# Kernel optimization log

Hardware: AMD Instinct MI355X
Metric: run time of the kernel (lower is better)

The kernel has to match this reference:

```python
import jax, jax.numpy as jnp
import numpy as np

EPS = 1e-5  # torch.nn.CosineSimilarity eps


def setup_inputs() -> dict:
    key = jax.random.key(0)
    x = jax.random.normal(key, (8, 256, 1024), dtype=jnp.float32)
    return {"batch_sequence_tensors": x}


def _worst_sim(x):
    # For every contiguous window [s, e] (1 <= s < e <= S-1, matching
    # exclude_special_tokens + sequential combinatorics), compute
    # min_t in [s,e] cos(mean(x[s:e+1]), x[t]).
    # Trick: dot(sum_{s..e} x_i, x_t) comes from a prefix sum of the Gram
    # matrix, and ||sum_{s..e} x||^2 from a 2-D prefix sum of the Gram matrix,
    # avoiding any [B,S,S,D] intermediates.
    B, S, D = x.shape
    G = jnp.einsum('bsd,btd->bst', x, x)  # [B,S,S] Gram

    # num[b,s,e,t] = sum_{i=s..e} x_i . x_t  via 1-D prefix sum over i
    Cpad = jnp.pad(jnp.cumsum(G, axis=1), ((0, 0), (1, 0), (0, 0)))  # [B,S+1,S]
    num = Cpad[:, 1:, :][:, None, :, :] - Cpad[:, :S, :][:, :, None, :]  # [B,S,S,S]

    # ||sum_{s..e} x||^2 = sum_{i,j in [s,e]} G[i,j] via 2-D prefix sum
    PP = jnp.pad(jnp.cumsum(jnp.cumsum(G, axis=1), axis=2),
                 ((0, 0), (1, 0), (1, 0)))  # [B,S+1,S+1]
    dE = jnp.diagonal(PP[:, 1:, 1:], axis1=1, axis2=2)   # PP[e+1,e+1]  [B,S]
    dS = jnp.diagonal(PP[:, :S, :S], axis1=1, axis2=2)   # PP[s,s]      [B,S]
    cross1 = PP[:, :S, 1:]                               # PP[s,e+1]  axes (s,e)
    cross2 = jnp.swapaxes(PP[:, 1:, :S], 1, 2)           # PP[e+1,s] -> (s,e)
    ssq = dE[:, None, :] + dS[:, :, None] - cross1 - cross2  # [B,S,S]
    sum_norm = jnp.sqrt(jnp.maximum(ssq, 0.0))               # ||sum||

    idx = jnp.arange(S)
    win_len = jnp.maximum(idx[None, :] - idx[:, None] + 1, 1).astype(x.dtype)  # [S,S] (s,e)
    # center = sum / len ; cosine uses the mean exactly as the torch module
    mean_norm = sum_norm / win_len                       # [B,S,S]
    x_norm = jnp.sqrt(jnp.maximum(jnp.diagonal(G, axis1=1, axis2=2), 0.0))  # [B,S]
    denom = jnp.maximum(mean_norm[..., None] * x_norm[:, None, None, :], EPS)
    cos = (num / win_len[None, :, :, None]) / denom      # [B,S,S,S]

    t_in = (idx[None, None, :] >= idx[:, None, None]) & \
           (idx[None, None, :] <= idx[None, :, None])    # [S,S,S] (s,e,t)
    worst = jnp.min(jnp.where(t_in[None], cos, jnp.inf), axis=-1)  # [B,S,S]

    valid = (idx[:, None] >= 1) & (idx[None, :] > idx[:, None])    # 1<=s<e<=S-1
    return jnp.where(valid[None], worst, 0.0)


def reference(batch_sequence_tensors):
    # worst_sim[b,s,e] = min cosine similarity of window mean vs members;
    # the original module's group mask is worst_sim >= threshold (0.9),
    # followed by (data-dependent, non-tensor) subset removal.
    return _worst_sim(batch_sequence_tensors)
```

## Files before the change

### kernel.cpp

```cpp
#include <hip/hip_runtime.h>
#include <stdint.h>

#define NB 8
#define NS 256
#define ND 1024
#define EPSF 1e-5f
#define BIGF 3.0e38f

typedef __attribute__((ext_vector_type(8))) short short8;
typedef __attribute__((ext_vector_type(4))) float f32x4;

__device__ __forceinline__ unsigned short f2bf(float f) {
  unsigned int u = __float_as_uint(f);
  u = (u + 0x7FFFu + ((u >> 16) & 1u)) >> 16;
  return (unsigned short)u;
}

__global__ __launch_bounds__(256) void k_convert(const float* __restrict__ x,
                                                 unsigned short* __restrict__ xb, int n4) {
  int idx = blockIdx.x * blockDim.x + threadIdx.x;
  int stride = gridDim.x * blockDim.x;
  for (int i = idx; i < n4; i += stride) {
    float4 v = reinterpret_cast<const float4*>(x)[i];
    ushort4 o;
    o.x = f2bf(v.x); o.y = f2bf(v.y); o.z = f2bf(v.z); o.w = f2bf(v.w);
    reinterpret_cast<ushort4*>(xb)[i] = o;
  }
}

__global__ __launch_bounds__(256) void k_gemm(const unsigned short* __restrict__ xb,
                                              float* __restrict__ gp) {
  int gw = ((blockIdx.x << 8) + threadIdx.x) >> 6;
  int lane = threadIdx.x & 63;
  int b  = gw & 7;
  int mt = (gw >> 3) & 7;
  int nt = (gw >> 6) & 7;
  int ks = gw >> 9;
  const unsigned short* Ab = xb + ((size_t)b << 18) + ((size_t)(mt << 5) << 10);
  const unsigned short* Bb = xb + ((size_t)b << 18) + ((size_t)(nt << 5) << 10);
  int lr = lane & 15;
  int lk = (lane >> 4) << 3;
  f32x4 acc00 = {0.f,0.f,0.f,0.f}, acc01 = {0.f,0.f,0.f,0.f};
  f32x4 acc10 = {0.f,0.f,0.f,0.f}, acc11 = {0.f,0.f,0.f,0.f};
  int kbase = (ks << 8) + lk;
#pragma unroll 2
  for (int kk = 0; kk < 256; kk += 32) {
    int ko = kbase + kk;
    short8 a0  = *reinterpret_cast<const short8*>(Ab + ((size_t)lr << 10) + ko);
    short8 a1  = *reinterpret_cast<const short8*>(Ab + ((size_t)(16 + lr) << 10) + ko);
    short8 bb0 = *reinterpret_cast<const short8*>(Bb + ((size_t)lr << 10) + ko);
    short8 bb1 = *reinterpret_cast<const short8*>(Bb + ((size_t)(16 + lr) << 10) + ko);
    acc00 = __builtin_amdgcn_mfma_f32_16x16x32_bf16(a0, bb0, acc00, 0, 0, 0);
    acc01 = __builtin_amdgcn_mfma_f32_16x16x32_bf16(a0, bb1, acc01, 0, 0, 0);
    acc10 = __builtin_amdgcn_mfma_f32_16x16x32_bf16(a1, bb0, acc10, 0, 0, 0);
    acc11 = __builtin_amdgcn_mfma_f32_16x16x32_bf16(a1, bb1, acc11, 0, 0, 0);
  }
  float* G = gp + (size_t)ks * (NB * NS * NS) + (size_t)b * NS * NS;
  int r0 = (mt << 5) + ((lane >> 4) << 2);
  int c0 = (nt << 5) + lr;
#pragma unroll
  for (int j = 0; j < 4; ++j) {
    G[(r0 + j) * NS + c0]           = acc00[j];
    G[(r0 + j) * NS + c0 + 16]      = acc01[j];
    G[(r0 + 16 + j) * NS + c0]      = acc10[j];
    G[(r0 + 16 + j) * NS + c0 + 16] = acc11[j];
  }
}

__global__ __launch_bounds__(64) void k_prefix(const float* __restrict__ gp, float* __restrict__ C,
                                               float* __restrict__ DGa, float* __restrict__ IXa) {
  int b = blockIdx.x >> 2;
  int t = ((blockIdx.x & 3) << 6) + threadIdx.x;
  const float* g = gp + (size_t)b * NS * NS;
  const int NP = NB * NS * NS;
  float* Cb = C + (size_t)b * 257 * NS;
  float run = 0.f, mydg = 0.f;
  Cb[t] = 0.f;
  for (int j = 0; j < NS; ++j) {
    int o = j * NS + t;
    float gv = g[o] + g[NP + o] + g[2 * NP + o] + g[3 * NP + o];
    if (j == t) mydg = gv;
    run += gv;
    Cb[(j + 1) * NS + t] = run;
  }
  DGa[b * NS + t] = mydg;
  float xn = sqrtf(fmaxf(mydg, 0.f));
  IXa[b * NS + t] = 1.0f / xn;
}

__global__ __launch_bounds__(256) void k_scan(const float* __restrict__ C, float* __restrict__ S2) {
  int id = blockIdx.x * 4 + (threadIdx.x >> 6);
  int lane = threadIdx.x & 63;
  int b = id / 257;
  int r = id - b * 257;
  const float* Crow = C + ((size_t)b * 257 + r) * NS;
  float* Srow = S2 + ((size_t)b * 257 + r) * 257;
  if (lane == 0) Srow[0] = 0.f;
  float run = 0.f;
  for (int c0 = 0; c0 < NS; c0 += 64) {
    float v = Crow[c0 + lane];
#pragma unroll
    for (int off = 1; off < 64; off <<= 1) {
      float n = __shfl_up(v, off);
      if (lane >= off) v += n;
    }
    Srow[c0 + lane + 1] = run + v;
    run += __shfl(v, 63);
  }
}

__global__ __launch_bounds__(64) void k_wmax(const float* __restrict__ IXa, float* __restrict__ WM) {
  int b = blockIdx.x;
  int lane = threadIdx.x;
  const float* IXb = IXa + b * NS;
  float m = 0.f;
#pragma unroll
  for (int k = 0; k < 4; ++k) m = fmaxf(m, IXb[k * 64 + lane]);
#pragma unroll
  for (int off = 32; off; off >>= 1) m = fmaxf(m, __shfl_xor(m, off));
  if (lane == 0) WM[b] = m;
}

static __device__ const unsigned char kTi[20] = {0,0,0,0,1,1,1,1,2,2,2,3,3,3,4,4,5,5,6,7};
static __device__ const unsigned char kTj[20] = {0,1,2,3,0,1,2,3,1,2,3,1,2,3,2,3,2,3,3,3};

__global__ __launch_bounds__(256) void k_trop(const float* __restrict__ C,
                                              const float* __restrict__ S2,
                                              const float* __restrict__ IXa,
                                              const float* __restrict__ DGa,
                                              const float* __restrict__ WM,
                                              float* __restrict__ out) {
  __shared__ float As[64][36];
  __shared__ float Bs[64][68];
  int blk = blockIdx.x;
  int b = blk / 20;
  int tix = blk - b * 20;
  int i0 = (int)kTi[tix] * 32;
  int j0 = (int)kTj[tix] * 64;
  int tid = threadIdx.x;
  int ii0 = (tid >> 4) << 1;
  int jj0 = (tid & 15) << 2;
  const float* Cb = C + (size_t)b * 257 * NS;
  const float* IXb = IXa + b * NS;
  float acc[8];
#pragma unroll
  for (int k = 0; k < 8; ++k) acc[k] = BIGF;

  int rA = tid >> 4;
  int c4 = (tid & 15) << 2;

  for (int t0 = i0 & ~63; t0 < j0 + 64; t0 += 64) {
    __syncthreads();
    float4 wv = *reinterpret_cast<const float4*>(IXb + t0 + c4);
#pragma unroll
    for (int p = 0; p < 2; ++p) {
      int r = i0 + p * 16 + rA;
      float4 v = *reinterpret_cast<const float4*>(Cb + (size_t)r * NS + t0 + c4);
      As[c4 + 0][p * 16 + rA] = v.x * wv.x;
      As[c4 + 1][p * 16 + rA] = v.y * wv.y;
      As[c4 + 2][p * 16 + rA] = v.z * wv.z;
      As[c4 + 3][p * 16 + rA] = v.w * wv.w;
    }
#pragma unroll
    for (int p = 0; p < 4; ++p) {
      int r = j0 + 1 + p * 16 + rA;
      float4 v = *reinterpret_cast<const float4*>(Cb + (size_t)r * NS + t0 + c4);
      Bs[c4 + 0][p * 16 + rA] = v.x * wv.x;
      Bs[c4 + 1][p * 16 + rA] = v.y * wv.y;
      Bs[c4 + 2][p * 16 + rA] = v.z * wv.z;
      Bs[c4 + 3][p * 16 + rA] = v.w * wv.w;
    }
    __syncthreads();

    int thA = i0 + ii0 - t0;
    int thB = j0 + jj0 - t0;
    if (thA <= -1 && thB >= 63) {
#pragma unroll 4
      for (int tt = 0; tt < 64; ++tt) {
        float2 a = *reinterpret_cast<const float2*>(&As[tt][ii0]);
        float4 bv = *reinterpret_cast<const float4*>(&Bs[tt][jj0]);
        acc[0] = fminf(acc[0], bv.x - a.x);
        acc[1] = fminf(acc[1], bv.y - a.x);
        acc[2] = fminf(acc[2], bv.z - a.x);
        acc[3] = fminf(acc[3], bv.w - a.x);
        acc[4] = fminf(acc[4], bv.x - a.y);
        acc[5] = fminf(acc[5], bv.y - a.y);
        acc[6] = fminf(acc[6], bv.z - a.y);
        acc[7] = fminf(acc[7], bv.w - a.y);
      }
    } else {
#pragma unroll 4
      for (int tt = 0; tt < 64; ++tt) {
        float2 a = *reinterpret_cast<const float2*>(&As[tt][ii0]);
        float4 bv = *reinterpret_cast<const float4*>(&Bs[tt][jj0]);
        float a0 = (tt >= thA)     ? a.x  : -BIGF;
        float a1 = (tt >= thA + 1) ? a.y  : -BIGF;
        float b0 = (tt <= thB)     ? bv.x :  BIGF;
        float b1 = (tt <= thB + 1) ? bv.y :  BIGF;
        float b2 = (tt <= thB + 2) ? bv.z :  BIGF;
        float b3 = (tt <= thB + 3) ? bv.w :  BIGF;
        acc[0] = fminf(acc[0], b0 - a0);
        acc[1] = fminf(acc[1], b1 - a0);
        acc[2] = fminf(acc[2], b2 - a0);
        acc[3] = fminf(acc[3], b3 - a0);
        acc[4] = fminf(acc[4], b0 - a1);
        acc[5] = fminf(acc[5], b1 - a1);
        acc[6] = fminf(acc[6], b2 - a1);
        acc[7] = fminf(acc[7], b3 - a1);
      }
    }
  }

  const float* S2b = S2 + (size_t)b * 257 * 257;
  const float* DGb = DGa + b * NS;
  float wmb = WM[b];
  float* outb = out + ((size_t)b << 16);
#pragma unroll
  for (int k = 0; k < 2; ++k) {
    int i = i0 + ii0 + k;
    if (i < 1) continue;
    float s2ii = S2b[(size_t)i * 257 + i];
#pragma unroll
    for (int l = 0; l < 4; ++l) {
      int j = j0 + jj0 + l;
      if (j <= i) continue;
      float s2jj = S2b[(size_t)(j + 1) * 257 + (j + 1)];
      float s2ij = S2b[(size_t)i * 257 + (j + 1)];
      float s2ji = S2b[(size_t)(j + 1) * 257 + i];
      float ssq = (s2jj - s2ij) - (s2ji - s2ii);
      float sn = sqrtf(fmaxf(ssq, 0.f));
      float win = (float)(j - i + 1);
      float res;
      if (sn >= EPSF * win * wmb) {
        res = acc[k * 4 + l] / sn;
      } else {
        float mn = sn / win;
        float m = BIGF;
        const float* r2 = Cb + (size_t)(j + 1) * NS;
        const float* r1 = Cb + (size_t)i * NS;
        for (int t = i; t <= j; ++t) {
          float num = r2[t] - r1[t];
          float xn = sqrtf(fmaxf(DGb[t], 0.f));
          float den = fmaxf(mn * xn, EPSF);
          m = fminf(m, num / win / den);
        }
        res = m;
      }
      outb[(size_t)i * NS + j] = res;
    }
  }
}

extern "C" void kernel_launch(void* const* d_in, const int* in_sizes, int n_in,
                              void* d_out, int out_size, void* d_ws, size_t ws_size,
                              hipStream_t stream) {
  (void)in_sizes; (void)n_in; (void)ws_size;
  const float* x = (const float*)d_in[0];
  float* out = (float*)d_out;
  char* ws = (char*)d_ws;
  unsigned short* Xb = (unsigned short*)(ws);
  float* Gp  = (float*)(ws + 4194304);
  float* C   = (float*)(ws + 12582912);
  float* S2  = (float*)(ws + 14688256);
  float* DGa = (float*)(ws + 16801824);
  float* IXa = (float*)(ws + 16810016);
  float* WM  = (float*)(ws + 16818208);

  hipMemsetAsync(d_out, 0, (size_t)out_size * sizeof(float), stream);
  k_convert<<<1024, 256, 0, stream>>>(x, Xb, (NB * NS * ND) / 4);
  k_gemm<<<512, 256, 0, stream>>>(Xb, Gp);
  k_prefix<<<32, 64, 0, stream>>>(Gp, C, DGa, IXa);
  k_scan<<<514, 256, 0, stream>>>(C, S2);
  k_wmax<<<8, 64, 0, stream>>>(IXa, WM);
  k_trop<<<160, 256, 0, stream>>>(C, S2, IXa, DGa, WM, out);
}
```

Measured before the change: 127.3 us.

## Compute prefix-sum Gram directly via GEMM of prefix-summed X, fuse auxiliary kernels

Replaces the Gram-then-column-prefix pipeline with a prefix sum over the sequence of X in bf16 (Y), then a GEMM Y·X^T that yields the prefix Gram directly. This removes the serial k_prefix kernel. Row norms move into the convert kernel, the weight max moves into k_trop, and the output memset is replaced by explicit zero writes in lower-triangle tiles. The GEMM split-K drops from 4 to 2. Rounding the running prefix sum to bf16 loses precision on large accumulated sums, and the new k_ypfx is a serial scan over 256 rows done by only 32 blocks.

```diff
diff --git a/kernel.cpp b/kernel.cpp
--- a/kernel.cpp
+++ b/kernel.cpp
@@ -15,36 +15,67 @@
   u = (u + 0x7FFFu + ((u >> 16) & 1u)) >> 16;
   return (unsigned short)u;
 }
+__device__ __forceinline__ float bf2f(unsigned short u) {
+  return __uint_as_float((unsigned int)u << 16);
+}
 
 __global__ __launch_bounds__(256) void k_convert(const float* __restrict__ x,
-                                                 unsigned short* __restrict__ xb, int n4) {
-  int idx = blockIdx.x * blockDim.x + threadIdx.x;
-  int stride = gridDim.x * blockDim.x;
-  for (int i = idx; i < n4; i += stride) {
-    float4 v = reinterpret_cast<const float4*>(x)[i];
-    ushort4 o;
-    o.x = f2bf(v.x); o.y = f2bf(v.y); o.z = f2bf(v.z); o.w = f2bf(v.w);
-    reinterpret_cast<ushort4*>(xb)[i] = o;
-  }
-}
-
-__global__ __launch_bounds__(256) void k_gemm(const unsigned short* __restrict__ xb,
-                                              float* __restrict__ gp) {
+                                                 unsigned short* __restrict__ xb,
+                                                 float* __restrict__ DGa,
+                                                 float* __restrict__ IXa) {
+  int row = blockIdx.x * 4 + (threadIdx.x >> 6);
+  int lane = threadIdx.x & 63;
+  size_t base = (size_t)row * ND;
+  float sq = 0.f;
+#pragma unroll
+  for (int c = 0; c < 4; ++c) {
+    size_t o = base + c * 256 + lane * 4;
+    float4 v = *reinterpret_cast<const float4*>(x + o);
+    ushort4 ob;
+    ob.x = f2bf(v.x); ob.y = f2bf(v.y); ob.z = f2bf(v.z); ob.w = f2bf(v.w);
+    *reinterpret_cast<ushort4*>(xb + o) = ob;
+    sq += v.x * v.x + v.y * v.y + v.z * v.z + v.w * v.w;
+  }
+#pragma unroll
+  for (int off = 32; off; off >>= 1) sq += __shfl_xor(sq, off);
+  if (lane == 0) {
+    DGa[row] = sq;
+    IXa[row] = 1.0f / sqrtf(sq);
+  }
+}
+
+__global__ __launch_bounds__(256) void k_ypfx(const unsigned short* __restrict__ xb,
+                                              unsigned short* __restrict__ yb) {
+  int gid = blockIdx.x * 256 + threadIdx.x;
+  int b = gid >> 10;
+  int d = gid & 1023;
+  const unsigned short* xr = xb + ((size_t)b << 18) + d;
+  unsigned short* yr = yb + ((size_t)b << 18) + d;
+  float run = 0.f;
+  for (int s = 0; s < NS; ++s) {
+    run += bf2f(xr[(size_t)s * ND]);
+    yr[(size_t)s * ND] = f2bf(run);
+  }
+}
+
+__global__ __launch_bounds__(256) void k_gemmC(const unsigned short* __restrict__ yb,
+                                               const unsigned short* __restrict__ xb,
+                                               float* __restrict__ cp) {
   int gw = ((blockIdx.x << 8) + threadIdx.x) >> 6;
   int lane = threadIdx.x & 63;
   int b  = gw & 7;
   int mt = (gw >> 3) & 7;
   int nt = (gw >> 6) & 7;
-  int ks = gw >> 9;
-  const unsigned short* Ab = xb + ((size_t)b << 18) + ((size_t)(mt << 5) << 10);
+  int ks = (gw >> 9) & 1;
+  const unsigned short* Ab = yb + ((size_t)b << 18) + ((size_t)(mt << 5) << 10);
   const unsigned short* Bb = xb + ((size_t)b << 18) + ((size_t)(nt << 5) << 10);
   int lr = lane & 15;
   int lk = (lane >> 4) << 3;
   f32x4 acc00 = {0.f,0.f,0.f,0.f}, acc01 = {0.f,0.f,0.f,0.f};
   f32x4 acc10 = {0.f,0.f,0.f,0.f}, acc11 = {0.f,0.f,0.f,0.f};
-  int kbase = (ks << 8) + lk;
+  int kbase = (ks << 9) + lk;
 #pragma unroll 2
-  for (int kk = 0; kk < 256; kk += 32) {
+  for (int kk = 0; kk < 512; kk += 32) {
     int ko = kbase + kk;
     short8 a0  = *reinterpret_cast<const short8*>(Ab + ((size_t)lr << 10) + ko);
     short8 a1  = *reinterpret_cast<const short8*>(Ab + ((size_t)(16 + lr) << 10) + ko);
@@ -55,7 +86,7 @@
     acc10 = __builtin_amdgcn_mfma_f32_16x16x32_bf16(a1, bb0, acc10, 0, 0, 0);
     acc11 = __builtin_amdgcn_mfma_f32_16x16x32_bf16(a1, bb1, acc11, 0, 0, 0);
   }
-  float* G = gp + (size_t)ks * (NB * NS * NS) + (size_t)b * NS * NS;
+  float* G = cp + (size_t)ks * (NB * NS * NS) + ((size_t)b << 16);
   int r0 = (mt << 5) + ((lane >> 4) << 2);
   int c0 = (nt << 5) + lr;
 #pragma unroll
@@ -67,38 +98,22 @@
   }
 }
 
-__global__ __launch_bounds__(64) void k_prefix(const float* __restrict__ gp, float* __restrict__ C,
-                                               float* __restrict__ DGa, float* __restrict__ IXa) {
-  int b = blockIdx.x >> 2;
-  int t = ((blockIdx.x & 3) << 6) + threadIdx.x;
-  const float* g = gp + (size_t)b * NS * NS;
-  const int NP = NB * NS * NS;
-  float* Cb = C + (size_t)b * 257 * NS;
-  float run = 0.f, mydg = 0.f;
-  Cb[t] = 0.f;
-  for (int j = 0; j < NS; ++j) {
-    int o = j * NS + t;
-    float gv = g[o] + g[NP + o] + g[2 * NP + o] + g[3 * NP + o];
-    if (j == t) mydg = gv;
-    run += gv;
-    Cb[(j + 1) * NS + t] = run;
-  }
-  DGa[b * NS + t] = mydg;
-  float xn = sqrtf(fmaxf(mydg, 0.f));
-  IXa[b * NS + t] = 1.0f / xn;
-}
-
-__global__ __launch_bounds__(256) void k_scan(const float* __restrict__ C, float* __restrict__ S2) {
+__global__ __launch_bounds__(256) void k_scan(const float* __restrict__ cp,
+                                              float* __restrict__ C, float* __restrict__ S2) {
   int id = blockIdx.x * 4 + (threadIdx.x >> 6);
   int lane = threadIdx.x & 63;
   int b = id / 257;
   int r = id - b * 257;
-  const float* Crow = C + ((size_t)b * 257 + r) * NS;
+  float* Crow = C + ((size_t)b * 257 + r) * NS;
   float* Srow = S2 + ((size_t)b * 257 + r) * 257;
+  const float* p0 = cp + (((size_t)b << 8) + (r - 1)) * NS;
+  const float* p1 = p0 + (size_t)NB * NS * NS;
   if (lane == 0) Srow[0] = 0.f;
   float run = 0.f;
   for (int c0 = 0; c0 < NS; c0 += 64) {
-    float v = Crow[c0 + lane];
+    float v = 0.f;
+    if (r > 0) v = p0[c0 + lane] + p1[c0 + lane];
+    Crow[c0 + lane] = v;
 #pragma unroll
     for (int off = 1; off < 64; off <<= 1) {
       float n = __shfl_up(v, off);
@@ -108,40 +123,43 @@
     run += __shfl(v, 63);
   }
 }
-
-__global__ __launch_bounds__(64) void k_wmax(const float* __restrict__ IXa, float* __restrict__ WM) {
-  int b = blockIdx.x;
-  int lane = threadIdx.x;
-  const float* IXb = IXa + b * NS;
-  float m = 0.f;
-#pragma unroll
-  for (int k = 0; k < 4; ++k) m = fmaxf(m, IXb[k * 64 + lane]);
-#pragma unroll
-  for (int off = 32; off; off >>= 1) m = fmaxf(m, __shfl_xor(m, off));
-  if (lane == 0) WM[b] = m;
-}
-
-static __device__ const unsigned char kTi[20] = {0,0,0,0,1,1,1,1,2,2,2,3,3,3,4,4,5,5,6,7};
-static __device__ const unsigned char kTj[20] = {0,1,2,3,0,1,2,3,1,2,3,1,2,3,2,3,2,3,3,3};
 
 __global__ __launch_bounds__(256) void k_trop(const float* __restrict__ C,
                                               const float* __restrict__ S2,
                                               const float* __restrict__ IXa,
                                               const float* __restrict__ DGa,
-                                              const float* __restrict__ WM,
                                               float* __restrict__ out) {
   __shared__ float As[64][36];
   __shared__ float Bs[64][68];
+  __shared__ float wred[4];
   int blk = blockIdx.x;
-  int b = blk / 20;
-  int tix = blk - b * 20;
-  int i0 = (int)kTi[tix] * 32;
-  int j0 = (int)kTj[tix] * 64;
+  int b = blk >> 5;
+  int tix = blk & 31;
+  int i0 = (tix >> 2) << 5;
+  int j0 = (tix & 3) << 6;
   int tid = threadIdx.x;
+  float* outb = out + ((size_t)b << 16);
+
+  if (i0 >= j0 + 63) {
+    float4 z = {0.f, 0.f, 0.f, 0.f};
+    float* p = outb + (size_t)(i0 + (tid >> 3)) * NS + j0 + ((tid & 7) << 3);
+    reinterpret_cast<float4*>(p)[0] = z;
+    reinterpret_cast<float4*>(p)[1] = z;
+    return;
+  }
+
+  const float* Cb = C + (size_t)b * 257 * NS;
+  const float* IXb = IXa + b * NS;
+
+  float wv0 = IXb[tid];
+#pragma unroll
+  for (int off = 32; off; off >>= 1) wv0 = fmaxf(wv0, __shfl_xor(wv0, off));
+  if ((tid & 63) == 0) wred[tid >> 6] = wv0;
+  __syncthreads();
+  float wmb = fmaxf(fmaxf(wred[0], wred[1]), fmaxf(wred[2], wred[3]));
+
   int ii0 = (tid >> 4) << 1;
   int jj0 = (tid & 15) << 2;
-  const float* Cb = C + (size_t)b * 257 * NS;
-  const float* IXb = IXa + b * NS;
   float acc[8];
 #pragma unroll
   for (int k = 0; k < 8; ++k) acc[k] = BIGF;
@@ -213,64 +231,63 @@
 
   const float* S2b = S2 + (size_t)b * 257 * 257;
   const float* DGb = DGa + b * NS;
-  float wmb = WM[b];
-  float* outb = out + ((size_t)b << 16);
 #pragma unroll
   for (int k = 0; k < 2; ++k) {
     int i = i0 + ii0 + k;
-    if (i < 1) continue;
+    float o4[4];
     float s2ii = S2b[(size_t)i * 257 + i];
 #pragma unroll
     for (int l = 0; l < 4; ++l) {
       int j = j0 + jj0 + l;
-      if (j <= i) continue;
-      float s2jj = S2b[(size_t)(j + 1) * 257 + (j + 1)];
-      float s2ij = S2b[(size_t)i * 257 + (j + 1)];
-      float s2ji = S2b[(size_t)(j + 1) * 257 + i];
-      float ssq = (s2jj - s2ij) - (s2ji - s2ii);
-      float sn = sqrtf(fmaxf(ssq, 0.f));
-      float win = (float)(j - i + 1);
-      float res;
-      if (sn >= EPSF * win * wmb) {
-        res = acc[k * 4 + l] / sn;
-      } else {
-        float mn = sn / win;
-        float m = BIGF;
-        const float* r2 = Cb + (size_t)(j + 1) * NS;
-        const float* r1 = Cb + (size_t)i * NS;
-        for (int t = i; t <= j; ++t) {
-          float num = r2[t] - r1[t];
-          float xn = sqrtf(fmaxf(DGb[t], 0.f));
-          float den = fmaxf(mn * xn, EPSF);
-          m = fminf(m, num / win / den);
+      float res = 0.f;
+      if (i >= 1 && j > i) {
+        float s2jj = S2b[(size_t)(j + 1) * 257 + (j + 1)];
+        float s2ij = S2b[(size_t)i * 257 + (j + 1)];
+        float s2ji = S2b[(size_t)(j + 1) * 257 + i];
+        float ssq = (s2jj - s2ij) - (s2ji - s2ii);
+        float sn = sqrtf(fmaxf(ssq, 0.f));
+        float win = (float)(j - i + 1);
+        if (sn >= EPSF * win * wmb) {
+          res = acc[k * 4 + l] / sn;
+        } else {
+          float mn = sn / win;
+          float m = BIGF;
+          const float* r2 = Cb + (size_t)(j + 1) * NS;
+          const float* r1 = Cb + (size_t)i * NS;
+          for (int t = i; t <= j; ++t) {
+            float num = r2[t] - r1[t];
+            float xn = sqrtf(fmaxf(DGb[t], 0.f));
+            float den = fmaxf(mn * xn, EPSF);
+            m = fminf(m, num / win / den);
+          }
+          res = m;
         }
-        res = m;
       }
-      outb[(size_t)i * NS + j] = res;
-    }
+      o4[l] = res;
+    }
+    float4 st = {o4[0], o4[1], o4[2], o4[3]};
+    *reinterpret_cast<float4*>(outb + (size_t)i * NS + j0 + jj0) = st;
   }
 }
 
 extern "C" void kernel_launch(void* const* d_in, const int* in_sizes, int n_in,
                               void* d_out, int out_size, void* d_ws, size_t ws_size,
                               hipStream_t stream) {
-  (void)in_sizes; (void)n_in; (void)ws_size;
+  (void)in_sizes; (void)n_in; (void)ws_size; (void)out_size;
   const float* x = (const float*)d_in[0];
   float* out = (float*)d_out;
   char* ws = (char*)d_ws;
   unsigned short* Xb = (unsigned short*)(ws);
-  float* Gp  = (float*)(ws + 4194304);
+  unsigned short* Yb = (unsigned short*)(ws + 4194304);
+  float* Cp  = (float*)(ws + 8388608);
   float* C   = (float*)(ws + 12582912);
   float* S2  = (float*)(ws + 14688256);
   float* DGa = (float*)(ws + 16801824);
   float* IXa = (float*)(ws + 16810016);
-  float* WM  = (float*)(ws + 16818208);
-
-  hipMemsetAsync(d_out, 0, (size_t)out_size * sizeof(float), stream);
-  k_convert<<<1024, 256, 0, stream>>>(x, Xb, (NB * NS * ND) / 4);
-  k_gemm<<<512, 256, 0, stream>>>(Xb, Gp);
-  k_prefix<<<32, 64, 0, stream>>>(Gp, C, DGa, IXa);
-  k_scan<<<514, 256, 0, stream>>>(C, S2);
-  k_wmax<<<8, 64, 0, stream>>>(IXa, WM);
-  k_trop<<<160, 256, 0, stream>>>(C, S2, IXa, DGa, WM, out);
-}
+
+  k_convert<<<512, 256, 0, stream>>>(x, Xb, DGa, IXa);
+  k_ypfx<<<32, 256, 0, stream>>>(Xb, Yb);
+  k_gemmC<<<256, 256, 0, stream>>>(Yb, Xb, Cp);
+  k_scan<<<514, 256, 0, stream>>>(Cp, C, S2);
+  k_trop<<<256, 256, 0, stream>>>(C, S2, IXa, DGa, out);
+}
```

Result: faster. 113.1 us (-11.1%).
